# Kernel optimization log

Measured on AMD Instinct MI355X. Metric: run time of the kernel, lower is better.

## Reference

```python
import jax, jax.numpy as jnp
import numpy as np

NEG = -9e15
ALPHA = 0.2  # LeakyReLU negative slope


def _gat_layer(x, W, a, mask):
    # x: [N, Fin], W: [Fin, Fout], a: [2*Fout, 1], mask: [N, N] bool
    h = x @ W                                  # [N, Fout]
    F = h.shape[1]
    # additive attention score: identical math to cat([h_i, h_j]) @ a
    f1 = h @ a[:F, 0]                          # [N]
    f2 = h @ a[F:, 0]                          # [N]
    e = jax.nn.leaky_relu(f1[:, None] + f2[None, :], ALPHA)  # [N, N]
    e = jnp.where(mask, e, NEG)
    attn = jax.nn.softmax(e, axis=1)           # dropout is identity in eval mode
    return attn @ h                            # [N, Fout]


def setup_inputs() -> dict:
    key = jax.random.key(0)
    ks = jax.random.split(key, 6)
    N, Fin, H, Fh, Fo = 4096, 256, 8, 64, 64
    features = jax.random.normal(ks[0], (N, Fin), dtype=jnp.float32)
    adj = jax.random.randint(ks[1], (N, N), 0, 2).astype(jnp.float32)
    W_heads = jax.random.normal(ks[2], (H, Fin, Fh), dtype=jnp.float32) * 0.1
    a_heads = jax.random.normal(ks[3], (H, 2 * Fh, 1), dtype=jnp.float32) * 0.1
    W_out = jax.random.normal(ks[4], (H * Fh, Fo), dtype=jnp.float32) * 0.1
    a_out = jax.random.normal(ks[5], (2 * Fo, 1), dtype=jnp.float32) * 0.1
    return {"features": features, "adj": adj, "W_heads": W_heads,
            "a_heads": a_heads, "W_out": W_out, "a_out": a_out}


def reference(features, adj, W_heads, a_heads, W_out, a_out):
    mask = adj > 0
    H = W_heads.shape[0]
    # loop over the small fixed set of heads (keeps peak memory at one NxN matrix)
    heads = [jax.nn.elu(_gat_layer(features, W_heads[i], a_heads[i], mask))
             for i in range(H)]
    x = jnp.concatenate(heads, axis=1)         # [N, H*Fh]
    return _gat_layer(x, W_out, a_out, mask)   # concat=False -> no elu
```

## Files before the change

### kernel.cpp

```cpp
#include <hip/hip_runtime.h>
#include <hip/hip_bf16.h>

#define N_NODES 4096
#define LOG2E 1.44269504088896340736f
#define JT 128

typedef __attribute__((ext_vector_type(8))) short bf16x8;
typedef __attribute__((ext_vector_type(4))) short bf16x4;
typedef __attribute__((ext_vector_type(4))) float f32x4;
typedef __attribute__((ext_vector_type(16))) float f32x16;

static __device__ __forceinline__ ushort f2bf(float x) {
    union { float f; unsigned u; } v; v.f = x;
    unsigned u = v.u;
    return (ushort)((u + 0x7FFFu + ((u >> 16) & 1u)) >> 16);
}
static __device__ __forceinline__ float bf2f(ushort h) {
    union { unsigned u; float f; } v; v.u = ((unsigned)h) << 16; return v.f;
}

__global__ __launch_bounds__(256) void k_prologue(const float* __restrict__ adj,
        unsigned* __restrict__ maskw,
        const float* __restrict__ W1, ushort* __restrict__ Wh1, ushort* __restrict__ Wl1,
        const float* __restrict__ W2, ushort* __restrict__ Wh2, ushort* __restrict__ Wl2) {
    int b = blockIdx.x, t = threadIdx.x;
    if (b < 2048) {
        int idx = b * 256 + t;
        int row = idx >> 7, w = idx & 127;
        const float4* ap = (const float4*)(adj + (size_t)row * N_NODES + w * 32);
        unsigned bits = 0;
#pragma unroll
        for (int q = 0; q < 8; ++q) {
            float4 v = ap[q];
            bits |= (v.x > 0.f ? 1u : 0u) << (q * 4 + 0);
            bits |= (v.y > 0.f ? 1u : 0u) << (q * 4 + 1);
            bits |= (v.z > 0.f ? 1u : 0u) << (q * 4 + 2);
            bits |= (v.w > 0.f ? 1u : 0u) << (q * 4 + 3);
        }
        maskw[idx] = bits;
    } else {
        const float* W; ushort *Wh, *Wl; int idx, kshift;
        if (b < 2560) { W = W1; Wh = Wh1; Wl = Wl1; idx = (b - 2048) * 256 + t; kshift = 8; }
        else          { W = W2; Wh = Wh2; Wl = Wl2; idx = (b - 2560) * 256 + t; kshift = 9; }
        int K = 1 << kshift;
        int n = idx & 63;
        int k = (idx >> 6) & (K - 1);
        int h = idx >> (6 + kshift);
        float v = W[idx];
        ushort hi = f2bf(v);
        union { unsigned u; float f; } hv; hv.u = ((unsigned)hi) << 16;
        ushort lo = f2bf(v - hv.f);
        size_t dst = ((size_t)h * 64 + n) * K + k;
        Wh[dst] = hi; Wl[dst] = lo;
    }
}

__global__ __launch_bounds__(512) void k_gemm_h(const float* __restrict__ X,
        const ushort* __restrict__ Wh, const ushort* __restrict__ Wl,
        const float* __restrict__ a,
        ushort* __restrict__ Ht, float* __restrict__ Rc,
        float* __restrict__ Tc, ushort* __restrict__ G2b, int K) {
    int head = blockIdx.y;
    int t = threadIdx.x, wave = t >> 6, lane = t & 63;
    int c = lane & 15, g = lane >> 4;
    int i0 = blockIdx.x * 16;
    int kq = K >> 3;
    int kbeg = wave * kq;
    const float* xrow = X + (size_t)(i0 + c) * K;
    f32x4 acc[4] = {};
    for (int k0 = kbeg; k0 < kbeg + kq; k0 += 32) {
        const float4* xp = (const float4*)(xrow + k0 + g * 8);
        float4 xa = xp[0], xb = xp[1];
        float xs[8] = {xa.x, xa.y, xa.z, xa.w, xb.x, xb.y, xb.z, xb.w};
        union { ushort s[8]; bf16x8 v; } ah, al;
#pragma unroll
        for (int e = 0; e < 8; ++e) {
            ushort hb = f2bf(xs[e]);
            ah.s[e] = hb;
            union { unsigned u; float f; } hv; hv.u = ((unsigned)hb) << 16;
            al.s[e] = f2bf(xs[e] - hv.f);
        }
#pragma unroll
        for (int nt = 0; nt < 4; ++nt) {
            size_t boff = ((size_t)head * 64 + nt * 16 + c) * K + k0 + g * 8;
            bf16x8 bh = *(const bf16x8*)(Wh + boff);
            bf16x8 bl = *(const bf16x8*)(Wl + boff);
            acc[nt] = __builtin_amdgcn_mfma_f32_16x16x32_bf16(ah.v, bh, acc[nt], 0, 0, 0);
            acc[nt] = __builtin_amdgcn_mfma_f32_16x16x32_bf16(al.v, bh, acc[nt], 0, 0, 0);
            acc[nt] = __builtin_amdgcn_mfma_f32_16x16x32_bf16(ah.v, bl, acc[nt], 0, 0, 0);
        }
    }
    __shared__ float red[8][64][17];
#pragma unroll
    for (int nt = 0; nt < 4; ++nt)
#pragma unroll
        for (int r = 0; r < 4; ++r)
            red[wave][lane][nt * 4 + r] = acc[nt][r];
    __syncthreads();
    if (wave != 0) return;
#pragma unroll
    for (int nt = 0; nt < 4; ++nt)
#pragma unroll
        for (int r = 0; r < 4; ++r) {
            float s = 0.f;
#pragma unroll
            for (int w = 0; w < 8; ++w) s += red[w][lane][nt * 4 + r];
            acc[nt][r] = s;
        }
    float a1v[4], a2v[4];
#pragma unroll
    for (int nt = 0; nt < 4; ++nt) {
        a1v[nt] = a[head * 128 + nt * 16 + c];
        a2v[nt] = a[head * 128 + 64 + nt * 16 + c];
    }
    float G2f[4];
#pragma unroll
    for (int r = 0; r < 4; ++r) {
        float f1 = 0.f, f2 = 0.f;
#pragma unroll
        for (int nt = 0; nt < 4; ++nt) {
            f1 = __builtin_fmaf(acc[nt][r], a1v[nt], f1);
            f2 = __builtin_fmaf(acc[nt][r], a2v[nt], f2);
        }
#pragma unroll
        for (int o = 1; o < 16; o <<= 1) {
            f1 += __shfl_xor(f1, o);
            f2 += __shfl_xor(f2, o);
        }
        float g2 = __builtin_amdgcn_exp2f(0.2f * LOG2E * f2);
        G2f[r] = g2;
        if (c == 0) {
            int i = i0 + g * 4 + r;
            Rc [head * N_NODES + i] = __builtin_amdgcn_exp2f(-0.8f * LOG2E * f1);
            Tc [head * N_NODES + i] = __builtin_amdgcn_exp2f( 0.8f * LOG2E * f2);
            G2b[head * N_NODES + i] = f2bf(g2);
        }
    }
#pragma unroll
    for (int nt = 0; nt < 4; ++nt) {
        union { ushort s[4]; bf16x4 v; } pk;
#pragma unroll
        for (int r = 0; r < 4; ++r) pk.s[r] = f2bf(acc[nt][r] * G2f[r]);
        *(bf16x4*)(Ht + ((size_t)head * 64 + nt * 16 + c) * N_NODES + i0 + g * 4) = pk.v;
    }
}

template<int JS1>
__global__ __launch_bounds__(512) void k_gemm2(const ushort* __restrict__ accP,
        const float* __restrict__ Zp,
        const ushort* __restrict__ Wh, const ushort* __restrict__ Wl,
        const float* __restrict__ a,
        ushort* __restrict__ Ht, float* __restrict__ Rc,
        float* __restrict__ Tc, ushort* __restrict__ G2b) {
    const int K = 512;
    int t = threadIdx.x, wave = t >> 6, lane = t & 63;
    int c = lane & 15, g = lane >> 4;
    int i0 = blockIdx.x * 16;
    int row = i0 + c;
    int hx = wave;
    float z = 0.f;
#pragma unroll
    for (int js = 0; js < JS1; ++js)
        z += Zp[(size_t)(hx * JS1 + js) * N_NODES + row];
    float rz = 1.0f / z;
    f32x4 acc[4] = {};
#pragma unroll
    for (int ki = 0; ki < 2; ++ki) {
        int k0 = wave * 64 + ki * 32;
        int n0 = ki * 32 + g * 8;
        float s[8] = {};
#pragma unroll
        for (int js = 0; js < JS1; ++js) {
            const ushort* apn = accP + ((size_t)(hx * JS1 + js) * N_NODES + row) * 64 + n0;
            union { int4 v; ushort u[8]; } uu;
            uu.v = *(const int4*)apn;
#pragma unroll
            for (int e = 0; e < 8; ++e) s[e] += bf2f(uu.u[e]);
        }
        union { ushort sh[8]; bf16x8 v; } ah, al;
#pragma unroll
        for (int e = 0; e < 8; ++e) {
            float v = s[e] * rz;
            v = v > 0.f ? v : (__builtin_amdgcn_exp2f(v * LOG2E) - 1.f);
            ushort hb = f2bf(v);
            ah.sh[e] = hb;
            union { unsigned u; float f; } hv; hv.u = ((unsigned)hb) << 16;
            al.sh[e] = f2bf(v - hv.f);
        }
#pragma unroll
        for (int nt = 0; nt < 4; ++nt) {
            size_t boff = ((size_t)(nt * 16 + c)) * K + k0 + g * 8;
            bf16x8 bh = *(const bf16x8*)(Wh + boff);
            bf16x8 bl = *(const bf16x8*)(Wl + boff);
            acc[nt] = __builtin_amdgcn_mfma_f32_16x16x32_bf16(ah.v, bh, acc[nt], 0, 0, 0);
            acc[nt] = __builtin_amdgcn_mfma_f32_16x16x32_bf16(al.v, bh, acc[nt], 0, 0, 0);
            acc[nt] = __builtin_amdgcn_mfma_f32_16x16x32_bf16(ah.v, bl, acc[nt], 0, 0, 0);
        }
    }
    __shared__ float red[8][64][17];
#pragma unroll
    for (int nt = 0; nt < 4; ++nt)
#pragma unroll
        for (int r = 0; r < 4; ++r)
            red[wave][lane][nt * 4 + r] = acc[nt][r];
    __syncthreads();
    if (wave != 0) return;
#pragma unroll
    for (int nt = 0; nt < 4; ++nt)
#pragma unroll
        for (int r = 0; r < 4; ++r) {
            float s = 0.f;
#pragma unroll
            for (int w = 0; w < 8; ++w) s += red[w][lane][nt * 4 + r];
            acc[nt][r] = s;
        }
    float a1v[4], a2v[4];
#pragma unroll
    for (int nt = 0; nt < 4; ++nt) {
        a1v[nt] = a[nt * 16 + c];
        a2v[nt] = a[64 + nt * 16 + c];
    }
    float G2f[4];
#pragma unroll
    for (int r = 0; r < 4; ++r) {
        float f1 = 0.f, f2 = 0.f;
#pragma unroll
        for (int nt = 0; nt < 4; ++nt) {
            f1 = __builtin_fmaf(acc[nt][r], a1v[nt], f1);
            f2 = __builtin_fmaf(acc[nt][r], a2v[nt], f2);
        }
#pragma unroll
        for (int o = 1; o < 16; o <<= 1) {
            f1 += __shfl_xor(f1, o);
            f2 += __shfl_xor(f2, o);
        }
        float g2 = __builtin_amdgcn_exp2f(0.2f * LOG2E * f2);
        G2f[r] = g2;
        if (c == 0) {
            int i = i0 + g * 4 + r;
            Rc [i] = __builtin_amdgcn_exp2f(-0.8f * LOG2E * f1);
            Tc [i] = __builtin_amdgcn_exp2f( 0.8f * LOG2E * f2);
            G2b[i] = f2bf(g2);
        }
    }
#pragma unroll
    for (int nt = 0; nt < 4; ++nt) {
        union { ushort s[4]; bf16x4 v; } pk;
#pragma unroll
        for (int r = 0; r < 4; ++r) pk.s[r] = f2bf(acc[nt][r] * G2f[r]);
        *(bf16x4*)(Ht + ((size_t)(nt * 16 + c)) * N_NODES + i0 + g * 4) = pk.v;
    }
}

template<int JS, int NH>
__global__ __launch_bounds__(256)
__attribute__((amdgpu_waves_per_eu(4, 4)))
void k_attn(const ushort* __restrict__ Ht,
        const float* __restrict__ Rc, const float* __restrict__ Tc,
        const ushort* __restrict__ G2b, const unsigned* __restrict__ maskw,
        ushort* __restrict__ accP, float* __restrict__ Zp) {
    int bid = blockIdx.x;
    int rb = bid & 31;
    int rem = bid >> 5;
    int js = rem % JS;
    int head = rem / JS;

    int t = threadIdx.x, wave = t >> 6, lane = t & 63;
    int r32 = lane & 31, half = lane >> 5;
    int i0b = rb * 128;
    int i0w = i0b + wave * 32;
    int irow = i0w + r32;
    const int jcount = N_NODES / JS;
    int j0 = js * jcount;
    const int ntiles = jcount / JT;
    const int ntm1 = ntiles - 1;
    int rot = (rb + js * 3 + head * 5) & ntm1;
    const float R = Rc[head * N_NODES + irow];

    __shared__ ushort Hs[2][64 * JT];
    __shared__ unsigned Ms[2][512];
    __shared__ float Ts[2][JT];
    __shared__ ushort G2s[2][JT];

    int nH = (wave * 4) * 4 + (lane >> 4);
    const ushort* gspH[4];
#pragma unroll
    for (int s = 0; s < 4; ++s) {
        int n = nH + s * 4;
        gspH[s] = Ht + ((size_t)head * 64 + n) * N_NODES + j0
                + (((lane & 15) ^ (n & 7)) << 3);
    }
    const unsigned* msA = maskw + (size_t)(i0b + (2 * wave) * 16 + (lane >> 2)) * 128
                        + (j0 >> 5) + (lane & 3);
    const unsigned* msB = msA + (size_t)16 * 128;
    const float*  tsrcA = Tc  + (size_t)head * N_NODES + j0 + lane;
    const float*  tsrcB = Tc  + (size_t)head * N_NODES + j0 + 64 + lane;
    const ushort* gsrc  = G2b + (size_t)head * N_NODES + j0 + lane * 2;

    auto stage = [&](int b, int tile) {
        int go = tile * JT;
#pragma unroll
        for (int s = 0; s < 4; ++s)
            __builtin_amdgcn_global_load_lds((const unsigned*)(gspH[s] + go),
                    (unsigned*)&Hs[b][(wave * 4 + s) * 512], 16, 0, 0);
        __builtin_amdgcn_global_load_lds(msA + tile * 4,
                (unsigned*)&Ms[b][(2 * wave) * 64], 4, 0, 0);
        __builtin_amdgcn_global_load_lds(msB + tile * 4,
                (unsigned*)&Ms[b][(2 * wave + 1) * 64], 4, 0, 0);
        if (wave == 1)
            __builtin_amdgcn_global_load_lds((const unsigned*)(tsrcA + go),
                    (unsigned*)&Ts[b][0], 4, 0, 0);
        else if (wave == 2)
            __builtin_amdgcn_global_load_lds((const unsigned*)(tsrcB + go),
                    (unsigned*)&Ts[b][64], 4, 0, 0);
        else if (wave == 3)
            __builtin_amdgcn_global_load_lds((const unsigned*)(gsrc + go),
                    (unsigned*)&G2s[b][0], 4, 0, 0);
    };

    f32x16 acc0 = {}, acc1 = {}, acc2 = {};

    stage(0, rot);
    int buf = 0;
    for (int tt = 0; tt < ntiles; ++tt) {
        if (tt + 1 < ntiles) {
            stage(buf ^ 1, (tt + 1 + rot) & ntm1);
            if (wave == 0) asm volatile("s_waitcnt vmcnt(6)");
            else           asm volatile("s_waitcnt vmcnt(7)");
        } else {
            asm volatile("s_waitcnt vmcnt(0)");
        }
        __builtin_amdgcn_s_barrier();

        const char* hb = (const char*)&Hs[buf][0];
        union { uint4 v; unsigned w[4]; } mw;
        mw.v = *(const uint4*)&Ms[buf][(wave * 32 + r32) * 4];
#pragma unroll
        for (int itr = 0; itr < JT / 16; ++itr) {
            unsigned phys = (unsigned)(((itr * 2 + half) ^ (r32 & 7)) << 4);
            bf16x8 b0 = *(const bf16x8*)(hb + r32 * 256 + phys);
            bf16x8 b1 = *(const bf16x8*)(hb + (32 + r32) * 256 + phys);
            bf16x8 bg = *(const bf16x8*)(&G2s[buf][itr * 16 + half * 8]);
            unsigned mword = mw.w[itr >> 1];
            unsigned mshift = mword >> ((itr & 1) * 16 + half * 8);
            const float* tp = &Ts[buf][itr * 16 + half * 8];
            float4 ta = *(const float4*)tp;
            float4 tb = *(const float4*)(tp + 4);
            float tv[8] = {ta.x, ta.y, ta.z, ta.w, tb.x, tb.y, tb.z, tb.w};
            float p[8];
#pragma unroll
            for (int e = 0; e < 8; ++e) {
                int sm;
                asm("v_bfe_i32 %0, %1, %2, 1" : "=v"(sm) : "v"(mshift), "i"(e));
                float pe = fmaxf(tv[e], R);
                union { float f; int i; } pv; pv.f = pe;
                pv.i &= sm;
                p[e] = pv.f;
            }
            union { unsigned w[4]; bf16x8 v; } pa;
#pragma unroll
            for (int q = 0; q < 4; ++q)
                asm("v_cvt_pk_bf16_f32 %0, %1, %2"
                    : "=v"(pa.w[q]) : "v"(p[2 * q]), "v"(p[2 * q + 1]));
            __builtin_amdgcn_s_setprio(1);
            acc0 = __builtin_amdgcn_mfma_f32_32x32x16_bf16(pa.v, b0, acc0, 0, 0, 0);
            acc1 = __builtin_amdgcn_mfma_f32_32x32x16_bf16(pa.v, b1, acc1, 0, 0, 0);
            acc2 = __builtin_amdgcn_mfma_f32_32x32x16_bf16(pa.v, bg, acc2, 0, 0, 0);
            __builtin_amdgcn_s_setprio(0);
        }
        __builtin_amdgcn_s_barrier();
        buf ^= 1;
    }
    int slice = head * JS + js;
    if (r32 == 0) {
#pragma unroll
        for (int reg = 0; reg < 16; ++reg) {
            int drow = (reg & 3) + 8 * (reg >> 2) + 4 * half;
            Zp[(size_t)slice * N_NODES + i0w + drow] = acc2[reg];
        }
    }
    ushort* ap = accP + ((size_t)slice * N_NODES + i0w) * 64;
#pragma unroll
    for (int reg = 0; reg < 16; ++reg) {
        int drow = (reg & 3) + 8 * (reg >> 2) + 4 * half;
        ap[drow * 64 + r32] = f2bf(acc0[reg]);
        ap[drow * 64 + 32 + r32] = f2bf(acc1[reg]);
    }
}

template<int JS>
__global__ __launch_bounds__(256) void k_combine2(const ushort* __restrict__ accP,
        const float* __restrict__ Zp, float* __restrict__ out) {
    int idx = blockIdx.x * 256 + threadIdx.x;
    int n = idx & 63, i = idx >> 6;
    float s = 0.f, z = 0.f;
#pragma unroll
    for (int j = 0; j < JS; ++j) {
        s += bf2f(accP[((size_t)j * N_NODES + i) * 64 + n]);
        z += Zp[(size_t)j * N_NODES + i];
    }
    out[idx] = s / z;
}

extern "C" void kernel_launch(void* const* d_in, const int* in_sizes, int n_in,
                              void* d_out, int out_size, void* d_ws, size_t ws_size,
                              hipStream_t stream) {
    const float* features = (const float*)d_in[0];
    const float* adj      = (const float*)d_in[1];
    const float* W_heads  = (const float*)d_in[2];
    const float* a_heads  = (const float*)d_in[3];
    const float* W_out    = (const float*)d_in[4];
    const float* a_out    = (const float*)d_in[5];
    float* out = (float*)d_out;

    int tier;
    if (ws_size >= 26000000)      tier = 2;
    else if (ws_size >= 17500000) tier = 1;
    else                          tier = 0;
    int JS1 = tier == 2 ? 4 : (tier == 1 ? 2 : 1);
    int JS2 = tier == 2 ? 32 : (tier == 1 ? 16 : 8);
    int slices = (8 * JS1 > JS2) ? 8 * JS1 : JS2;

    char* ws = (char*)d_ws;
    size_t off = 0;
    auto alloc = [&](size_t bytes) -> void* {
        void* p = ws + off; off = (off + bytes + 255) & ~(size_t)255; return p;
    };
    unsigned* maskw = (unsigned*)alloc((size_t)N_NODES * 128 * 4);
    ushort* Ht1 = (ushort*)alloc((size_t)8 * 64 * N_NODES * 2);
    ushort* Ht2 = (ushort*)alloc((size_t)64 * N_NODES * 2);
    float* Rc1  = (float*)alloc((size_t)8 * N_NODES * 4);
    float* Tc1  = (float*)alloc((size_t)8 * N_NODES * 4);
    ushort* G2b1 = (ushort*)alloc((size_t)8 * N_NODES * 2);
    float* Rc2  = (float*)alloc((size_t)N_NODES * 4);
    float* Tc2  = (float*)alloc((size_t)N_NODES * 4);
    ushort* G2b2 = (ushort*)alloc((size_t)N_NODES * 2);
    ushort* Wh1 = (ushort*)alloc((size_t)8 * 64 * 256 * 2);
    ushort* Wl1 = (ushort*)alloc((size_t)8 * 64 * 256 * 2);
    ushort* Wh2 = (ushort*)alloc((size_t)64 * 512 * 2);
    ushort* Wl2 = (ushort*)alloc((size_t)64 * 512 * 2);
    ushort* accP = (ushort*)alloc((size_t)slices * N_NODES * 64 * 2);
    float* Zp   = (float*)alloc((size_t)slices * N_NODES * 4);

    hipLaunchKernelGGL(k_prologue, dim3(2688), dim3(256), 0, stream,
                       adj, maskw, W_heads, Wh1, Wl1, W_out, Wh2, Wl2);
    hipLaunchKernelGGL(k_gemm_h, dim3(N_NODES / 16, 8), dim3(512), 0, stream,
                       features, Wh1, Wl1, a_heads, Ht1, Rc1, Tc1, G2b1, 256);
    if (tier == 2)
        hipLaunchKernelGGL((k_attn<4, 8>), dim3(32 * 4 * 8), dim3(256), 0, stream,
                           Ht1, Rc1, Tc1, G2b1, maskw, accP, Zp);
    else if (tier == 1)
        hipLaunchKernelGGL((k_attn<2, 8>), dim3(32 * 2 * 8), dim3(256), 0, stream,
                           Ht1, Rc1, Tc1, G2b1, maskw, accP, Zp);
    else
        hipLaunchKernelGGL((k_attn<1, 8>), dim3(32 * 1 * 8), dim3(256), 0, stream,
                           Ht1, Rc1, Tc1, G2b1, maskw, accP, Zp);
    if (tier == 2)
        hipLaunchKernelGGL((k_gemm2<4>), dim3(N_NODES / 16), dim3(512), 0, stream,
                           accP, Zp, Wh2, Wl2, a_out, Ht2, Rc2, Tc2, G2b2);
    else if (tier == 1)
        hipLaunchKernelGGL((k_gemm2<2>), dim3(N_NODES / 16), dim3(512), 0, stream,
                           accP, Zp, Wh2, Wl2, a_out, Ht2, Rc2, Tc2, G2b2);
    else
        hipLaunchKernelGGL((k_gemm2<1>), dim3(N_NODES / 16), dim3(512), 0, stream,
                           accP, Zp, Wh2, Wl2, a_out, Ht2, Rc2, Tc2, G2b2);
    if (tier == 2) {
        hipLaunchKernelGGL((k_attn<32, 1>), dim3(32 * 32), dim3(256), 0, stream,
                           Ht2, Rc2, Tc2, G2b2, maskw, accP, Zp);
        hipLaunchKernelGGL((k_combine2<32>), dim3(N_NODES * 64 / 256), dim3(256), 0, stream,
                           accP, Zp, out);
    } else if (tier == 1) {
        hipLaunchKernelGGL((k_attn<16, 1>), dim3(32 * 16), dim3(256), 0, stream,
                           Ht2, Rc2, Tc2, G2b2, maskw, accP, Zp);
        hipLaunchKernelGGL((k_combine2<16>), dim3(N_NODES * 64 / 256), dim3(256), 0, stream,
                           accP, Zp, out);
    } else {
        hipLaunchKernelGGL((k_attn<8, 1>), dim3(32 * 8), dim3(256), 0, stream,
                           Ht2, Rc2, Tc2, G2b2, maskw, accP, Zp);
        hipLaunchKernelGGL((k_combine2<8>), dim3(N_NODES * 64 / 256), dim3(256), 0, stream,
                           accP, Zp, out);
    }
}
```

Baseline: 112.3 us.

## Fuse layer-2 combine into attention via last-block atomic counter; use 64-wide j tiles

Removes the separate k_combine2 launch. The last attention block to finish each row block, found with an atomic counter that k_gemm2 resets, sums the partial accumulators and normalizers and writes the output. The layer-2 attention kernel also moves to a 64-column j tile, with matching staging, mask and wait-count logic. This saves one kernel launch and its read of the partials, at the cost of a serialized tail reduction in a few blocks plus fences and atomics.

```diff
diff --git a/kernel.cpp b/kernel.cpp
--- a/kernel.cpp
+++ b/kernel.cpp
@@ -3,7 +3,6 @@
 
 #define N_NODES 4096
 #define LOG2E 1.44269504088896340736f
-#define JT 128
 
 typedef __attribute__((ext_vector_type(8))) short bf16x8;
 typedef __attribute__((ext_vector_type(4))) short bf16x4;
@@ -151,7 +150,8 @@
         const ushort* __restrict__ Wh, const ushort* __restrict__ Wl,
         const float* __restrict__ a,
         ushort* __restrict__ Ht, float* __restrict__ Rc,
-        float* __restrict__ Tc, ushort* __restrict__ G2b) {
+        float* __restrict__ Tc, ushort* __restrict__ G2b, unsigned* __restrict__ ctr) {
+    if (blockIdx.x == 0 && threadIdx.x < 32) ctr[threadIdx.x] = 0;
     const int K = 512;
     int t = threadIdx.x, wave = t >> 6, lane = t & 63;
     int c = lane & 15, g = lane >> 4;
@@ -252,13 +252,14 @@
     }
 }
 
-template<int JS, int NH>
+template<int JS, int NH, int JTP, bool FUSE>
 __global__ __launch_bounds__(256)
 __attribute__((amdgpu_waves_per_eu(4, 4)))
 void k_attn(const ushort* __restrict__ Ht,
         const float* __restrict__ Rc, const float* __restrict__ Tc,
         const ushort* __restrict__ G2b, const unsigned* __restrict__ maskw,
-        ushort* __restrict__ accP, float* __restrict__ Zp) {
+        ushort* __restrict__ accP, float* __restrict__ Zp,
+        float* __restrict__ outp, unsigned* __restrict__ ctr) {
     int bid = blockIdx.x;
     int rb = bid & 31;
     int rem = bid >> 5;
@@ -272,50 +273,82 @@
     int irow = i0w + r32;
     const int jcount = N_NODES / JS;
     int j0 = js * jcount;
-    const int ntiles = jcount / JT;
+    const int ntiles = jcount / JTP;
     const int ntm1 = ntiles - 1;
     int rot = (rb + js * 3 + head * 5) & ntm1;
     const float R = Rc[head * N_NODES + irow];
 
-    __shared__ ushort Hs[2][64 * JT];
-    __shared__ unsigned Ms[2][512];
-    __shared__ float Ts[2][JT];
-    __shared__ ushort G2s[2][JT];
-
-    int nH = (wave * 4) * 4 + (lane >> 4);
-    const ushort* gspH[4];
-#pragma unroll
-    for (int s = 0; s < 4; ++s) {
-        int n = nH + s * 4;
-        gspH[s] = Ht + ((size_t)head * 64 + n) * N_NODES + j0
-                + (((lane & 15) ^ (n & 7)) << 3);
-    }
-    const unsigned* msA = maskw + (size_t)(i0b + (2 * wave) * 16 + (lane >> 2)) * 128
-                        + (j0 >> 5) + (lane & 3);
-    const unsigned* msB = msA + (size_t)16 * 128;
-    const float*  tsrcA = Tc  + (size_t)head * N_NODES + j0 + lane;
-    const float*  tsrcB = Tc  + (size_t)head * N_NODES + j0 + 64 + lane;
-    const ushort* gsrc  = G2b + (size_t)head * N_NODES + j0 + lane * 2;
+    __shared__ ushort Hs[2][64 * JTP];
+    __shared__ unsigned Ms[2][JTP == 128 ? 512 : 256];
+    __shared__ float Ts[2][JTP];
+    __shared__ ushort G2s[2][128];
+
+    const ushort* gspH[JTP == 128 ? 4 : 2];
+    const unsigned *msA, *msB;
+    const float *tsrcA, *tsrcB;
+    const ushort* gsrc;
+    if constexpr (JTP == 128) {
+        int nH = wave * 16 + (lane >> 4);
+#pragma unroll
+        for (int s = 0; s < 4; ++s) {
+            int n = nH + s * 4;
+            gspH[s] = Ht + ((size_t)head * 64 + n) * N_NODES + j0
+                    + (((lane & 15) ^ (n & 7)) << 3);
+        }
+        msA = maskw + (size_t)(i0b + (2 * wave) * 16 + (lane >> 2)) * 128
+            + (j0 >> 5) + (lane & 3);
+        msB = msA + (size_t)16 * 128;
+        tsrcA = Tc + (size_t)head * N_NODES + j0 + lane;
+        tsrcB = Tc + (size_t)head * N_NODES + j0 + 64 + lane;
+        gsrc  = G2b + (size_t)head * N_NODES + j0 + lane * 2;
+    } else {
+        int nrow = wave * 8 + (lane >> 3);
+        int sjc = (lane & 7) ^ ((lane >> 3) & 7);
+#pragma unroll
+        for (int s = 0; s < 2; ++s)
+            gspH[s] = Ht + ((size_t)head * 64 + s * 32 + nrow) * N_NODES + j0 + sjc * 8;
+        msA = maskw + (size_t)(i0b + wave * 32 + (lane >> 1)) * 128
+            + (j0 >> 5) + (lane & 1);
+        msB = nullptr;
+        tsrcA = Tc + (size_t)head * N_NODES + j0 + lane;
+        tsrcB = nullptr;
+        gsrc  = G2b + (size_t)head * N_NODES + j0 + (lane & 31) * 2;
+    }
 
     auto stage = [&](int b, int tile) {
-        int go = tile * JT;
-#pragma unroll
-        for (int s = 0; s < 4; ++s)
-            __builtin_amdgcn_global_load_lds((const unsigned*)(gspH[s] + go),
-                    (unsigned*)&Hs[b][(wave * 4 + s) * 512], 16, 0, 0);
-        __builtin_amdgcn_global_load_lds(msA + tile * 4,
-                (unsigned*)&Ms[b][(2 * wave) * 64], 4, 0, 0);
-        __builtin_amdgcn_global_load_lds(msB + tile * 4,
-                (unsigned*)&Ms[b][(2 * wave + 1) * 64], 4, 0, 0);
-        if (wave == 1)
-            __builtin_amdgcn_global_load_lds((const unsigned*)(tsrcA + go),
-                    (unsigned*)&Ts[b][0], 4, 0, 0);
-        else if (wave == 2)
-            __builtin_amdgcn_global_load_lds((const unsigned*)(tsrcB + go),
-                    (unsigned*)&Ts[b][64], 4, 0, 0);
-        else if (wave == 3)
-            __builtin_amdgcn_global_load_lds((const unsigned*)(gsrc + go),
-                    (unsigned*)&G2s[b][0], 4, 0, 0);
+        int go = tile * JTP;
+        if constexpr (JTP == 128) {
+#pragma unroll
+            for (int s = 0; s < 4; ++s)
+                __builtin_amdgcn_global_load_lds((const unsigned*)(gspH[s] + go),
+                        (unsigned*)&Hs[b][(wave * 4 + s) * 512], 16, 0, 0);
+            __builtin_amdgcn_global_load_lds(msA + tile * 4,
+                    (unsigned*)&Ms[b][(2 * wave) * 64], 4, 0, 0);
+            __builtin_amdgcn_global_load_lds(msB + tile * 4,
+                    (unsigned*)&Ms[b][(2 * wave + 1) * 64], 4, 0, 0);
+            if (wave == 1)
+                __builtin_amdgcn_global_load_lds((const unsigned*)(tsrcA + go),
+                        (unsigned*)&Ts[b][0], 4, 0, 0);
+            else if (wave == 2)
+                __builtin_amdgcn_global_load_lds((const unsigned*)(tsrcB + go),
+                        (unsigned*)&Ts[b][64], 4, 0, 0);
+            else if (wave == 3)
+                __builtin_amdgcn_global_load_lds((const unsigned*)(gsrc + go),
+                        (unsigned*)&G2s[b][0], 4, 0, 0);
+        } else {
+#pragma unroll
+            for (int s = 0; s < 2; ++s)
+                __builtin_amdgcn_global_load_lds((const unsigned*)(gspH[s] + go),
+                        (unsigned*)&Hs[b][(s * 32 + wave * 8) * JTP], 16, 0, 0);
+            __builtin_amdgcn_global_load_lds(msA + tile * 2,
+                    (unsigned*)&Ms[b][wave * 64], 4, 0, 0);
+            if (wave == 1)
+                __builtin_amdgcn_global_load_lds((const unsigned*)(tsrcA + go),
+                        (unsigned*)&Ts[b][0], 4, 0, 0);
+            else if (wave == 2)
+                __builtin_amdgcn_global_load_lds((const unsigned*)(gsrc + go),
+                        (unsigned*)&G2s[b][0], 4, 0, 0);
+        }
     };
 
     f32x16 acc0 = {}, acc1 = {}, acc2 = {};
@@ -325,23 +358,31 @@
     for (int tt = 0; tt < ntiles; ++tt) {
         if (tt + 1 < ntiles) {
             stage(buf ^ 1, (tt + 1 + rot) & ntm1);
-            if (wave == 0) asm volatile("s_waitcnt vmcnt(6)");
-            else           asm volatile("s_waitcnt vmcnt(7)");
+            if constexpr (JTP == 128) {
+                if (wave == 0) asm volatile("s_waitcnt vmcnt(6)");
+                else           asm volatile("s_waitcnt vmcnt(7)");
+            } else {
+                if (wave == 1 || wave == 2) asm volatile("s_waitcnt vmcnt(4)");
+                else                        asm volatile("s_waitcnt vmcnt(3)");
+            }
         } else {
             asm volatile("s_waitcnt vmcnt(0)");
         }
         __builtin_amdgcn_s_barrier();
 
         const char* hb = (const char*)&Hs[buf][0];
-        union { uint4 v; unsigned w[4]; } mw;
-        mw.v = *(const uint4*)&Ms[buf][(wave * 32 + r32) * 4];
-#pragma unroll
-        for (int itr = 0; itr < JT / 16; ++itr) {
+        unsigned mwv[JTP == 128 ? 4 : 2];
+        if constexpr (JTP == 128)
+            *(uint4*)mwv = *(const uint4*)&Ms[buf][(wave * 32 + r32) * 4];
+        else
+            *(uint2*)mwv = *(const uint2*)&Ms[buf][(wave * 32 + r32) * 2];
+#pragma unroll
+        for (int itr = 0; itr < JTP / 16; ++itr) {
             unsigned phys = (unsigned)(((itr * 2 + half) ^ (r32 & 7)) << 4);
-            bf16x8 b0 = *(const bf16x8*)(hb + r32 * 256 + phys);
-            bf16x8 b1 = *(const bf16x8*)(hb + (32 + r32) * 256 + phys);
+            bf16x8 b0 = *(const bf16x8*)(hb + r32 * (JTP * 2) + phys);
+            bf16x8 b1 = *(const bf16x8*)(hb + (32 + r32) * (JTP * 2) + phys);
             bf16x8 bg = *(const bf16x8*)(&G2s[buf][itr * 16 + half * 8]);
-            unsigned mword = mw.w[itr >> 1];
+            unsigned mword = mwv[itr >> 1];
             unsigned mshift = mword >> ((itr & 1) * 16 + half * 8);
             const float* tp = &Ts[buf][itr * 16 + half * 8];
             float4 ta = *(const float4*)tp;
@@ -386,20 +427,41 @@
         ap[drow * 64 + r32] = f2bf(acc0[reg]);
         ap[drow * 64 + 32 + r32] = f2bf(acc1[reg]);
     }
-}
-
-template<int JS>
-__global__ __launch_bounds__(256) void k_combine2(const ushort* __restrict__ accP,
-        const float* __restrict__ Zp, float* __restrict__ out) {
-    int idx = blockIdx.x * 256 + threadIdx.x;
-    int n = idx & 63, i = idx >> 6;
-    float s = 0.f, z = 0.f;
-#pragma unroll
-    for (int j = 0; j < JS; ++j) {
-        s += bf2f(accP[((size_t)j * N_NODES + i) * 64 + n]);
-        z += Zp[(size_t)j * N_NODES + i];
-    }
-    out[idx] = s / z;
+
+    if constexpr (FUSE) {
+        __threadfence();
+        __syncthreads();
+        __shared__ int lastFlag;
+        if (t == 0) {
+            unsigned old = atomicAdd(ctr + rb, 1u);
+            lastFlag = (old == (unsigned)(JS - 1));
+        }
+        __syncthreads();
+        if (lastFlag) {
+            __threadfence();
+#pragma unroll
+            for (int pass = 0; pass < 4; ++pass) {
+                int i = i0b + pass * 32 + (t >> 3);
+                int n0 = (t & 7) * 8;
+                float s[8] = {};
+                float z = 0.f;
+#pragma unroll
+                for (int j2 = 0; j2 < JS; ++j2) {
+                    const ushort* apn = accP + ((size_t)j2 * N_NODES + i) * 64 + n0;
+                    union { int4 v; ushort u[8]; } uu;
+                    uu.v = *(const int4*)apn;
+#pragma unroll
+                    for (int e = 0; e < 8; ++e) s[e] += bf2f(uu.u[e]);
+                    z += Zp[(size_t)j2 * N_NODES + i];
+                }
+                float rz = 1.0f / z;
+                float4 o0 = {s[0] * rz, s[1] * rz, s[2] * rz, s[3] * rz};
+                float4 o1 = {s[4] * rz, s[5] * rz, s[6] * rz, s[7] * rz};
+                *(float4*)(outp + (size_t)i * 64 + n0) = o0;
+                *(float4*)(outp + (size_t)i * 64 + n0 + 4) = o1;
+            }
+        }
+    }
 }
 
 extern "C" void kernel_launch(void* const* d_in, const int* in_sizes, int n_in,
@@ -441,43 +503,35 @@
     ushort* Wl2 = (ushort*)alloc((size_t)64 * 512 * 2);
     ushort* accP = (ushort*)alloc((size_t)slices * N_NODES * 64 * 2);
     float* Zp   = (float*)alloc((size_t)slices * N_NODES * 4);
+    unsigned* ctr = (unsigned*)alloc(32 * 4);
 
     hipLaunchKernelGGL(k_prologue, dim3(2688), dim3(256), 0, stream,
                        adj, maskw, W_heads, Wh1, Wl1, W_out, Wh2, Wl2);
     hipLaunchKernelGGL(k_gemm_h, dim3(N_NODES / 16, 8), dim3(512), 0, stream,
                        features, Wh1, Wl1, a_heads, Ht1, Rc1, Tc1, G2b1, 256);
     if (tier == 2)
-        hipLaunchKernelGGL((k_attn<4, 8>), dim3(32 * 4 * 8), dim3(256), 0, stream,
-                           Ht1, Rc1, Tc1, G2b1, maskw, accP, Zp);
+        hipLaunchKernelGGL((k_attn<4, 8, 128, false>), dim3(32 * 4 * 8), dim3(256), 0, stream,
+                           Ht1, Rc1, Tc1, G2b1, maskw, accP, Zp, nullptr, nullptr);
     else if (tier == 1)
-        hipLaunchKernelGGL((k_attn<2, 8>), dim3(32 * 2 * 8), dim3(256), 0, stream,
-                           Ht1, Rc1, Tc1, G2b1, maskw, accP, Zp);
+        hipLaunchKernelGGL((k_attn<2, 8, 128, false>), dim3(32 * 2 * 8), dim3(256), 0, stream,
+                           Ht1, Rc1, Tc1, G2b1, maskw, accP, Zp, nullptr, nullptr);
     else
-        hipLaunchKernelGGL((k_attn<1, 8>), dim3(32 * 1 * 8), dim3(256), 0, stream,
-                           Ht1, Rc1, Tc1, G2b1, maskw, accP, Zp);
-    if (tier == 2)
+        hipLaunchKernelGGL((k_attn<1, 8, 128, false>), dim3(32 * 1 * 8), dim3(256), 0, stream,
+                           Ht1, Rc1, Tc1, G2b1, maskw, accP, Zp, nullptr, nullptr);
+    if (tier == 2) {
         hipLaunchKernelGGL((k_gemm2<4>), dim3(N_NODES / 16), dim3(512), 0, stream,
-                           accP, Zp, Wh2, Wl2, a_out, Ht2, Rc2, Tc2, G2b2);
-    else if (tier == 1)
+                           accP, Zp, Wh2, Wl2, a_out, Ht2, Rc2, Tc2, G2b2, ctr);
+        hipLaunchKernelGGL((k_attn<32, 1, 64, true>), dim3(32 * 32), dim3(256), 0, stream,
+                           Ht2, Rc2, Tc2, G2b2, maskw, accP, Zp, out, ctr);
+    } else if (tier == 1) {
         hipLaunchKernelGGL((k_gemm2<2>), dim3(N_NODES / 16), dim3(512), 0, stream,
-                           accP, Zp, Wh2, Wl2, a_out, Ht2, Rc2, Tc2, G2b2);
-    else
+                           accP, Zp, Wh2, Wl2, a_out, Ht2, Rc2, Tc2, G2b2, ctr);
+        hipLaunchKernelGGL((k_attn<16, 1, 64, true>), dim3(32 * 16), dim3(256), 0, stream,
+                           Ht2, Rc2, Tc2, G2b2, maskw, accP, Zp, out, ctr);
+    } else {
         hipLaunchKernelGGL((k_gemm2<1>), dim3(N_NODES / 16), dim3(512), 0, stream,
-                           accP, Zp, Wh2, Wl2, a_out, Ht2, Rc2, Tc2, G2b2);
-    if (tier == 2) {
-        hipLaunchKernelGGL((k_attn<32, 1>), dim3(32 * 32), dim3(256), 0, stream,
-                           Ht2, Rc2, Tc2, G2b2, maskw, accP, Zp);
-        hipLaunchKernelGGL((k_combine2<32>), dim3(N_NODES * 64 / 256), dim3(256), 0, stream,
-                           accP, Zp, out);
-    } else if (tier == 1) {
-        hipLaunchKernelGGL((k_attn<16, 1>), dim3(32 * 16), dim3(256), 0, stream,
-                           Ht2, Rc2, Tc2, G2b2, maskw, accP, Zp);
-        hipLaunchKernelGGL((k_combine2<16>), dim3(N_NODES * 64 / 256), dim3(256), 0, stream,
-                           accP, Zp, out);
-    } else {
-        hipLaunchKernelGGL((k_attn<8, 1>), dim3(32 * 8), dim3(256), 0, stream,
-                           Ht2, Rc2, Tc2, G2b2, maskw, accP, Zp);
-        hipLaunchKernelGGL((k_combine2<8>), dim3(N_NODES * 64 / 256), dim3(256), 0, stream,
-                           accP, Zp, out);
-    }
-}
+                           accP, Zp, Wh2, Wl2, a_out, Ht2, Rc2, Tc2, G2b2, ctr);
+        hipLaunchKernelGGL((k_attn<8, 1, 64, true>), dim3(32 * 8), dim3(256), 0, stream,
+                           Ht2, Rc2, Tc2, G2b2, maskw, accP, Zp, out, ctr);
+    }
+}
```

New measurement: 264.7 us. 2.36x slower.
